# Kernel tuning notes

Hardware: AMD Instinct MI355X
Metric: run time of the kernel (lower is better)

## Reference

```python
import jax, jax.numpy as jnp
import numpy as np

GROUP_SIZE = 64
SHARED_EXPERT_WEIGHT = 1.0
# FP4 E2M1 codebook: sign bit + {0,.5,1,1.5,2,3,4,6}
FP4_TABLE = jnp.array([0.0, 0.5, 1.0, 1.5, 2.0, 3.0, 4.0, 6.0,
                       -0.0, -0.5, -1.0, -1.5, -2.0, -3.0, -4.0, -6.0], dtype=jnp.float32)


def dequant_fp4(packed, scales, group_size=GROUP_SIZE):
    """packed: [..., K//8, N] int32 (8 nibbles along K per word),
    scales: [..., K//group_size, N] -> dequantized [..., K, N] fp32."""
    shifts = (jnp.arange(8, dtype=jnp.int32) * 4)[:, None]          # [8,1]
    nib = jnp.right_shift(packed[..., :, None, :], shifts) & 0xF     # [..., K//8, 8, N]
    w = FP4_TABLE[nib]
    K = packed.shape[-2] * 8
    w = w.reshape(packed.shape[:-2] + (K, packed.shape[-1]))         # [..., K, N]
    s = jnp.repeat(scales, group_size, axis=-2)                      # [..., K, N]
    return w * s


def setup_inputs() -> dict:
    key = jax.random.key(0)
    ks = jax.random.split(key, 12)
    T, K, I, E, TOPK = 2048, 2048, 1024, 8, 2
    GS = GROUP_SIZE
    MAXI = 2**31 - 1
    u = lambda k, shp: jax.random.uniform(k, shp, jnp.float32, 0.005, 0.02)
    probs = jax.random.uniform(ks[10], (T, TOPK), jnp.float32)
    probs = probs / probs.sum(-1, keepdims=True)
    return {
        "hidden_states": jax.random.normal(ks[0], (T, K), jnp.float32),
        "gate_up_weight_packed": jax.random.randint(ks[1], (E, K // 8, 2 * I), 0, MAXI, jnp.int32),
        "gate_up_scales": u(ks[2], (E, K // GS, 2 * I)),
        "down_weight_packed": jax.random.randint(ks[3], (E, I // 8, K), 0, MAXI, jnp.int32),
        "down_scales": u(ks[4], (E, I // GS, K)),
        "shared_gate_up_packed": jax.random.randint(ks[5], (K // 8, 2 * I), 0, MAXI, jnp.int32),
        "shared_gate_up_scales": u(ks[6], (K // GS, 2 * I)),
        "shared_down_packed": jax.random.randint(ks[7], (I // 8, K), 0, MAXI, jnp.int32),
        "shared_down_scales": u(ks[8], (I // GS, K)),
        "expert_ids": jax.random.randint(ks[9], (T, TOPK), 0, E, jnp.int32),
        "expert_probs": probs,
    }


def reference(hidden_states, gate_up_weight_packed, gate_up_scales,
              down_weight_packed, down_scales,
              shared_gate_up_packed, shared_gate_up_scales,
              shared_down_packed, shared_down_scales,
              expert_ids, expert_probs):
    x = hidden_states                                                # [T, K]
    E = gate_up_weight_packed.shape[0]
    # --- routed experts: dequant + grouped GEMM over all tokens per expert ---
    Wgu = dequant_fp4(gate_up_weight_packed, gate_up_scales)         # [E, K, 2I]
    Wd = dequant_fp4(down_weight_packed, down_scales)                # [E, I, K]
    h = jnp.einsum('tk,ekn->etn', x, Wgu)                            # [E, T, 2I]
    gate, up = jnp.split(h, 2, axis=-1)
    act = jax.nn.silu(gate) * up                                     # [E, T, I]
    y = jnp.einsum('eti,eik->etk', act, Wd)                          # [E, T, K]
    # combine[t,e] = sum over top-k slots routed to e of prob
    one_hot = jax.nn.one_hot(expert_ids, E, dtype=x.dtype)           # [T, topk, E]
    combine = jnp.einsum('tk,tke->te', expert_probs, one_hot)        # [T, E]
    out = jnp.einsum('te,etk->tk', combine, y)                       # [T, K]
    # --- shared expert (always applied, weighted) ---
    Wgu_s = dequant_fp4(shared_gate_up_packed, shared_gate_up_scales)  # [K, 2I]
    Wd_s = dequant_fp4(shared_down_packed, shared_down_scales)         # [I, K]
    hs = x @ Wgu_s
    gs, us = jnp.split(hs, 2, axis=-1)
    shared_out = (jax.nn.silu(gs) * us) @ Wd_s
    return out + SHARED_EXPERT_WEIGHT * shared_out
```

## Files before the change

### kernel.cpp

```cpp
#include <hip/hip_runtime.h>
#include <hip/hip_bf16.h>

#define T_TOK 2048
#define K_DIM 2048
#define I_DIM 1024
#define NE    8
#define TOPK  2
#define GS    64

#define NSLOT  (T_TOK * TOPK)
#define TOTROW (NSLOT + T_TOK)
#define MAXTILE 32

typedef __attribute__((ext_vector_type(8))) short short8;
typedef __attribute__((ext_vector_type(4))) float f32x4;

#define WS_XB   ((size_t)65536)
#define WS_ACT  (WS_XB  + (size_t)2048 * 2048 * 2)
#define WS_Y    (WS_ACT + (size_t)TOTROW * 1024 * 2)
#define WS_WGU  (WS_Y   + (size_t)TOTROW * 2048 * 2)
#define WS_WD   (WS_WGU + (size_t)9 * 2048 * 2048 * 2)


__device__ __forceinline__ unsigned pack2(float a, float b) {
    __hip_bfloat162 h = __float22bfloat162_rn(make_float2(a, b));
    return *reinterpret_cast<unsigned*>(&h);
}

__device__ __forceinline__ unsigned scale2(unsigned p, float s) {
    float f0 = __uint_as_float(p << 16) * s;
    float f1 = __uint_as_float(p & 0xFFFF0000u) * s;
    return pack2(f0, f1);
}

__device__ __forceinline__ float bf2f(ushort h) {
    return __uint_as_float((unsigned)h << 16);
}

__device__ __forceinline__ void dq_word(unsigned w, float s, unsigned o[4]) {
    unsigned lo  = w & 0x0F0F0F0Fu;
    unsigned hi  = (w >> 4) & 0x0F0F0F0Fu;
    unsigned mlo = lo & 0x07070707u, mhi = hi & 0x07070707u;
    unsigned Hlo = __builtin_amdgcn_perm(0x40404040u, 0x3F3F3F00u, mlo);
    unsigned Hhi = __builtin_amdgcn_perm(0x40404040u, 0x3F3F3F00u, mhi);
    unsigned Llo = __builtin_amdgcn_perm(0xC0804000u, 0xC0800000u, mlo);
    unsigned Lhi = __builtin_amdgcn_perm(0xC0804000u, 0xC0800000u, mhi);
    Hlo |= (lo & 0x08080808u) << 4;
    Hhi |= (hi & 0x08080808u) << 4;
    unsigned e01 = __builtin_amdgcn_perm(Hlo, Llo, 0x05010400u);
    unsigned e23 = __builtin_amdgcn_perm(Hlo, Llo, 0x07030602u);
    unsigned o01 = __builtin_amdgcn_perm(Hhi, Lhi, 0x05010400u);
    unsigned o23 = __builtin_amdgcn_perm(Hhi, Lhi, 0x07030602u);
    o[0] = scale2(e01, s); o[1] = scale2(e23, s);
    o[2] = scale2(o01, s); o[3] = scale2(o23, s);
}

__device__ __forceinline__ void gld16(const void* g, void* l) {
    __builtin_amdgcn_global_load_lds(
        (const __attribute__((address_space(1))) unsigned*)g,
        (__attribute__((address_space(3))) unsigned*)l, 16, 0, 0);
}

__global__ __launch_bounds__(256) void k_prep_route(
        const float* __restrict__ x, ushort* __restrict__ xb,
        const int* __restrict__ eids, const float* __restrict__ probs,
        int* __restrict__ gcnt, int* __restrict__ gbase,
        int* __restrict__ tok, int* __restrict__ inv) {
    int tid = threadIdx.x;
    int idx = blockIdx.x * 256 + tid;
    const float4* p = (const float4*)(x + (size_t)idx * 8);
    float4 f0 = p[0], f1 = p[1];
    unsigned u0 = pack2(f0.x, f0.z);
    unsigned u1 = pack2(f1.x, f1.z);
    unsigned u2 = pack2(f0.y, f0.w);
    unsigned u3 = pack2(f1.y, f1.w);
    *(int4*)(xb + (size_t)idx * 8) = make_int4(u0, u1, u2, u3);

    if (blockIdx.x == 0) {
        __shared__ int lcnt[NE], lbase[NE], lcur[NE];
        if (tid < NE) lcnt[tid] = 0;
        __syncthreads();
        for (int i = tid; i < NSLOT; i += 256)
            atomicAdd(&lcnt[eids[i]], 1);
        __syncthreads();
        if (tid == 0) {
            int acc = 0;
            for (int e = 0; e < NE; e++) { lbase[e] = acc; acc += lcnt[e]; }
        }
        __syncthreads();
        if (tid < NE) lcur[tid] = lbase[tid];
        __syncthreads();
        for (int i = tid; i < NSLOT; i += 256) {
            int e = eids[i];
            int pos = atomicAdd(&lcur[e], 1);
            tok[pos] = i >> 1;
            inv[i] = pos;
        }
        for (int t = tid; t < T_TOK; t += 256)
            tok[NSLOT + t] = t;
        if (tid < NE) { gcnt[tid] = lcnt[tid]; gbase[tid] = lbase[tid]; }
        if (tid == 0) { gcnt[NE] = T_TOK; gbase[NE] = NSLOT; }
    }
}

__global__ __launch_bounds__(256) void k_dq2(
        const int* __restrict__ gup, const float* __restrict__ gus,
        const int* __restrict__ sup, const float* __restrict__ sus,
        const int* __restrict__ dwp, const float* __restrict__ dsc,
        const int* __restrict__ sdp, const float* __restrict__ sds,
        ushort* __restrict__ wgu_t, ushort* __restrict__ wd_t) {
    int z = blockIdx.z;
    const int* wp; const float* sc; ushort* op; int KW;
    const int N = 2048;
    if (z < 9) {
        KW = 256;
        if (z < NE) { wp = gup + (size_t)z * KW * N; sc = gus + (size_t)z * (KW / 8) * N; }
        else        { wp = sup; sc = sus; }
        op = wgu_t + (size_t)z * KW * 8 * N;
    } else {
        KW = 128;
        int e = z - 9;
        if (blockIdx.x >= 16) return;
        if (e < NE) { wp = dwp + (size_t)e * KW * N; sc = dsc + (size_t)e * (KW / 8) * N; }
        else        { wp = sdp; sc = sds; }
        op = wd_t + (size_t)e * KW * 8 * N;
    }
    int kwt = blockIdx.x * 8 + threadIdx.x;
    int n   = blockIdx.y * 32 + threadIdx.y;
    unsigned w = (unsigned)wp[(size_t)kwt * N + n];
    float s = sc[(size_t)(kwt >> 3) * N + n];
    unsigned o[4]; dq_word(w, s, o);
    *(int4*)(op + (size_t)n * (KW * 8) + kwt * 8) = make_int4(o[0], o[1], o[2], o[3]);
}

__global__ __launch_bounds__(256) void k_gemm_gateup(
        const ushort* __restrict__ xb, const ushort* __restrict__ wgu_t,
        const int* __restrict__ gcnt, const int* __restrict__ gbase,
        const int* __restrict__ tokid, ushort* __restrict__ act) {
    int e = blockIdx.z, cnt = gcnt[e], m0 = blockIdx.y * 128;
    if (m0 >= cnt) return;
    int n0 = blockIdx.x * 64;
    int base = gbase[e];
    const ushort* wt = wgu_t + (size_t)e * 2048 * K_DIM;

    __shared__ __align__(16) ushort xs[128 * 64];
    __shared__ __align__(16) ushort bs[128 * 64];
    __shared__ int ltok[128];

    int tid = threadIdx.x;
    int lane = tid & 63, wv = tid >> 6;
    int lid = lane & 15, quad = lane >> 4;
    int wr = wv >> 1, wc = wv & 1;
    int l8 = lane >> 3, l7 = lane & 7;
    int chunk = (l7 ^ l8) * 8;

    if (tid < 128) ltok[tid] = (m0 + tid < cnt) ? tokid[base + m0 + tid] : 0;
    __syncthreads();

    const ushort* aSrc[4]; const ushort* bSrc[4];
    #pragma unroll
    for (int it = 0; it < 4; it++) {
        int rA = wv * 32 + it * 8 + l8;
        aSrc[it] = xb + (size_t)ltok[rA] * K_DIM + chunk;
        int h = rA >> 6, j = rA & 63;
        int col = (j < 32) ? (n0 + h * 32 + j) : (I_DIM + n0 + h * 32 + (j - 32));
        bSrc[it] = wt + (size_t)col * K_DIM + chunk;
    }

    f32x4 acc[4][4] = {};

    for (int k0 = 0; k0 < K_DIM; k0 += 64) {
        #pragma unroll
        for (int it = 0; it < 4; it++) {
            gld16(aSrc[it] + k0, &xs[(wv * 4 + it) * 512]);
            gld16(bSrc[it] + k0, &bs[(wv * 4 + it) * 512]);
        }
        __syncthreads();
        #pragma unroll
        for (int ks = 0; ks < 2; ks++) {
            int slot = ((ks * 4 + quad) ^ l7) * 8;
            short8 a[4], b[4];
            #pragma unroll
            for (int mt = 0; mt < 4; mt++)
                a[mt] = *(const short8*)&xs[(wr * 64 + mt * 16 + lid) * 64 + slot];
            #pragma unroll
            for (int nt = 0; nt < 4; nt++)
                b[nt] = *(const short8*)&bs[(wc * 64 + nt * 16 + lid) * 64 + slot];
            #pragma unroll
            for (int mt = 0; mt < 4; mt++)
                #pragma unroll
                for (int nt = 0; nt < 4; nt++)
                    acc[mt][nt] = __builtin_amdgcn_mfma_f32_16x16x32_bf16(
                        a[mt], b[nt], acc[mt][nt], 0, 0, 0);
        }
        __syncthreads();
    }

    int c7 = lid & 7;
    int delta = ((c7 >> 1) + ((c7 & 1) << 2)) - c7;
    #pragma unroll
    for (int mt = 0; mt < 4; mt++) {
        #pragma unroll
        for (int i = 0; i < 4; i++) {
            int row = wr * 64 + mt * 16 + quad * 4 + i;
            if (m0 + row < cnt) {
                size_t p = (size_t)(base + m0 + row);
                #pragma unroll
                for (int nt = 0; nt < 2; nt++) {
                    float g = acc[mt][nt][i], u = acc[mt][nt + 2][i];
                    float vv = g / (1.f + __expf(-g)) * u;
                    int ncol = n0 + wc * 32 + nt * 16 + lid;
                    __hip_bfloat16 hb = __float2bfloat16(vv);
                    act[p * I_DIM + ncol + delta] = *reinterpret_cast<ushort*>(&hb);
                }
            }
        }
    }
}

__global__ __launch_bounds__(256) void k_gemm_down(
        const ushort* __restrict__ actb, const ushort* __restrict__ wd_t,
        const int* __restrict__ gcnt, const int* __restrict__ gbase,
        ushort* __restrict__ y) {
    int e = blockIdx.z, cnt = gcnt[e], m0 = blockIdx.y * 128;
    if (m0 >= cnt) return;
    int n0 = blockIdx.x * 128;
    int base = gbase[e];
    const ushort* wt = wd_t + (size_t)e * 2048 * I_DIM;

    __shared__ __align__(16) ushort xs[128 * 64];
    __shared__ __align__(16) ushort bs[128 * 64];

    int tid = threadIdx.x;
    int lane = tid & 63, wv = tid >> 6;
    int lid = lane & 15, quad = lane >> 4;
    int wr = wv >> 1, wc = wv & 1;
    int l8 = lane >> 3, l7 = lane & 7;
    int chunk = (l7 ^ l8) * 8;

    const ushort* aSrc[4]; const ushort* bSrc[4];
    #pragma unroll
    for (int it = 0; it < 4; it++) {
        int rA = wv * 32 + it * 8 + l8;
        int rr = m0 + rA; if (rr >= cnt) rr = cnt - 1;
        aSrc[it] = actb + (size_t)(base + rr) * I_DIM + chunk;
        bSrc[it] = wt + (size_t)(n0 + rA) * I_DIM + chunk;
    }

    f32x4 acc[4][4] = {};

    for (int i0 = 0; i0 < I_DIM; i0 += 64) {
        #pragma unroll
        for (int it = 0; it < 4; it++) {
            gld16(aSrc[it] + i0, &xs[(wv * 4 + it) * 512]);
            gld16(bSrc[it] + i0, &bs[(wv * 4 + it) * 512]);
        }
        __syncthreads();
        #pragma unroll
        for (int ks = 0; ks < 2; ks++) {
            int slot = ((ks * 4 + quad) ^ l7) * 8;
            short8 a[4], b[4];
            #pragma unroll
            for (int mt = 0; mt < 4; mt++)
                a[mt] = *(const short8*)&xs[(wr * 64 + mt * 16 + lid) * 64 + slot];
            #pragma unroll
            for (int nt = 0; nt < 4; nt++)
                b[nt] = *(const short8*)&bs[(wc * 64 + nt * 16 + lid) * 64 + slot];
            #pragma unroll
            for (int mt = 0; mt < 4; mt++)
                #pragma unroll
                for (int nt = 0; nt < 4; nt++)
                    acc[mt][nt] = __builtin_amdgcn_mfma_f32_16x16x32_bf16(
                        a[mt], b[nt], acc[mt][nt], 0, 0, 0);
        }
        __syncthreads();
    }

    #pragma unroll
    for (int mt = 0; mt < 4; mt++) {
        #pragma unroll
        for (int i = 0; i < 4; i++) {
            int row = wr * 64 + mt * 16 + quad * 4 + i;
            if (m0 + row < cnt) {
                ushort* yrow = y + (size_t)(base + m0 + row) * 2048 + n0 + wc * 64 + lid;
                #pragma unroll
                for (int nt = 0; nt < 4; nt++) {
                    __hip_bfloat16 hb = __float2bfloat16(acc[mt][nt][i]);
                    yrow[nt * 16] = *reinterpret_cast<ushort*>(&hb);
                }
            }
        }
    }
}

__global__ __launch_bounds__(256) void k_combine(
        const ushort* __restrict__ y, const int* __restrict__ inv,
        const float* __restrict__ prb, float* __restrict__ out) {
    int idx = blockIdx.x * 256 + threadIdx.x;
    int t = idx >> 8;
    int c = (idx & 255) * 8;
    int p0 = inv[2 * t], p1 = inv[2 * t + 1];
    float w0 = prb[2 * t], w1 = prb[2 * t + 1];
    int4 a = *(const int4*)(y + (size_t)p0 * 2048 + c);
    int4 b = *(const int4*)(y + (size_t)p1 * 2048 + c);
    int4 s = *(const int4*)(y + (size_t)(NSLOT + t) * 2048 + c);
    const ushort* au = (const ushort*)&a;
    const ushort* bu = (const ushort*)&b;
    const ushort* su = (const ushort*)&s;
    float o[8];
    #pragma unroll
    for (int j = 0; j < 8; j++)
        o[j] = w0 * bf2f(au[j]) + w1 * bf2f(bu[j]) + bf2f(su[j]);
    *(float4*)(out + (size_t)t * 2048 + c)     = *(float4*)&o[0];
    *(float4*)(out + (size_t)t * 2048 + c + 4) = *(float4*)&o[4];
}

extern "C" void kernel_launch(void* const* d_in, const int* in_sizes, int n_in,
                              void* d_out, int out_size, void* d_ws, size_t ws_size,
                              hipStream_t stream) {
    const float* x    = (const float*)d_in[0];
    const int*   gup  = (const int*)d_in[1];
    const float* gus  = (const float*)d_in[2];
    const int*   dwp  = (const int*)d_in[3];
    const float* dsc  = (const float*)d_in[4];
    const int*   sup  = (const int*)d_in[5];
    const float* sus  = (const float*)d_in[6];
    const int*   sdp  = (const int*)d_in[7];
    const float* sds  = (const float*)d_in[8];
    const int*   eids = (const int*)d_in[9];
    const float* prb  = (const float*)d_in[10];
    float* out = (float*)d_out;

    char*   ws    = (char*)d_ws;
    int*    gcnt  = (int*)(ws + 0);
    int*    gbase = (int*)(ws + 64);
    int*    tok   = (int*)(ws + 128);
    int*    inv   = (int*)(ws + 24704);
    ushort* xb    = (ushort*)(ws + WS_XB);
    ushort* act   = (ushort*)(ws + WS_ACT);
    ushort* y     = (ushort*)(ws + WS_Y);
    ushort* wgu_t = (ushort*)(ws + WS_WGU);
    ushort* wd_t  = (ushort*)(ws + WS_WD);

    k_prep_route<<<(T_TOK * K_DIM / 8) / 256, 256, 0, stream>>>(
        x, xb, eids, prb, gcnt, gbase, tok, inv);
    k_dq2<<<dim3(32, 64, 18), dim3(8, 32), 0, stream>>>(
        gup, gus, sup, sus, dwp, dsc, sdp, sds, wgu_t, wd_t);
    k_gemm_gateup<<<dim3(I_DIM / 64, MAXTILE, NE + 1), 256, 0, stream>>>(
        xb, wgu_t, gcnt, gbase, tok, act);
    k_gemm_down<<<dim3(K_DIM / 128, MAXTILE, NE + 1), 256, 0, stream>>>(
        act, wd_t, gcnt, gbase, y);
    k_combine<<<(T_TOK * K_DIM / 8) / 256, 256, 0, stream>>>(y, inv, prb, out);
}
```

Baseline: 262.0 us.

## Merge prep and dequant kernels and compact GEMM grids via tile list

Fuses the bf16 conversion, routing and the FP4 weight dequantization into one front kernel, removing a launch and letting the independent pieces share one grid. The routing block now builds a compact list of (expert, m-offset) tiles so the grouped GEMMs launch a 2D grid of at most 55 items instead of 9x32 mostly-empty blocks. This cuts early-exit block scheduling overhead but adds an indirection read per block, and the single routing block still serializes its work inside the merged kernel.

```diff
diff --git a/kernel.cpp b/kernel.cpp
--- a/kernel.cpp
+++ b/kernel.cpp
@@ -10,7 +10,7 @@
 
 #define NSLOT  (T_TOK * TOPK)
 #define TOTROW (NSLOT + T_TOK)
-#define MAXTILE 32
+#define MAXITEM 55
 
 typedef __attribute__((ext_vector_type(8))) short short8;
 typedef __attribute__((ext_vector_type(4))) float f32x4;
@@ -61,22 +61,60 @@
         (__attribute__((address_space(3))) unsigned*)l, 16, 0, 0);
 }
 
-__global__ __launch_bounds__(256) void k_prep_route(
+#define GU_BLK  (9 * 2048)
+#define DN_BLK  (9 * 1024)
+#define PREP_BLK 2048
+#define FRONT_GRID (GU_BLK + DN_BLK + PREP_BLK + 1)
+
+__global__ __launch_bounds__(256) void k_front(
         const float* __restrict__ x, ushort* __restrict__ xb,
+        const int* __restrict__ gup, const float* __restrict__ gus,
+        const int* __restrict__ sup, const float* __restrict__ sus,
+        const int* __restrict__ dwp, const float* __restrict__ dsc,
+        const int* __restrict__ sdp, const float* __restrict__ sds,
+        ushort* __restrict__ wgu_t, ushort* __restrict__ wd_t,
         const int* __restrict__ eids, const float* __restrict__ probs,
         int* __restrict__ gcnt, int* __restrict__ gbase,
+        int* __restrict__ tileCnt, int* __restrict__ tileE, int* __restrict__ tileM,
         int* __restrict__ tok, int* __restrict__ inv) {
+    int id = blockIdx.x;
     int tid = threadIdx.x;
-    int idx = blockIdx.x * 256 + tid;
-    const float4* p = (const float4*)(x + (size_t)idx * 8);
-    float4 f0 = p[0], f1 = p[1];
-    unsigned u0 = pack2(f0.x, f0.z);
-    unsigned u1 = pack2(f1.x, f1.z);
-    unsigned u2 = pack2(f0.y, f0.w);
-    unsigned u3 = pack2(f1.y, f1.w);
-    *(int4*)(xb + (size_t)idx * 8) = make_int4(u0, u1, u2, u3);
-
-    if (blockIdx.x == 0) {
+
+    if (id < GU_BLK + DN_BLK) {
+        const int* wp; const float* sc; ushort* op; int KW, kwt;
+        const int N = 2048;
+        int tx = tid & 7, ty = tid >> 3;
+        int n;
+        if (id < GU_BLK) {
+            int e = id >> 11, rem = id & 2047;
+            int bx = rem & 31, by = rem >> 5;
+            KW = 256; kwt = bx * 8 + tx; n = by * 32 + ty;
+            if (e < NE) { wp = gup + (size_t)e * KW * N; sc = gus + (size_t)e * (KW / 8) * N; }
+            else        { wp = sup; sc = sus; }
+            op = wgu_t + (size_t)e * KW * 8 * N;
+        } else {
+            int id2 = id - GU_BLK;
+            int e = id2 >> 10, rem = id2 & 1023;
+            int bx = rem & 15, by = rem >> 4;
+            KW = 128; kwt = bx * 8 + tx; n = by * 32 + ty;
+            if (e < NE) { wp = dwp + (size_t)e * KW * N; sc = dsc + (size_t)e * (KW / 8) * N; }
+            else        { wp = sdp; sc = sds; }
+            op = wd_t + (size_t)e * KW * 8 * N;
+        }
+        unsigned w = (unsigned)wp[(size_t)kwt * N + n];
+        float s = sc[(size_t)(kwt >> 3) * N + n];
+        unsigned o[4]; dq_word(w, s, o);
+        *(int4*)(op + (size_t)n * (KW * 8) + kwt * 8) = make_int4(o[0], o[1], o[2], o[3]);
+    } else if (id < GU_BLK + DN_BLK + PREP_BLK) {
+        int idx = (id - GU_BLK - DN_BLK) * 256 + tid;
+        const float4* p = (const float4*)(x + (size_t)idx * 8);
+        float4 f0 = p[0], f1 = p[1];
+        unsigned u0 = pack2(f0.x, f0.z);
+        unsigned u1 = pack2(f1.x, f1.z);
+        unsigned u2 = pack2(f0.y, f0.w);
+        unsigned u3 = pack2(f1.y, f1.w);
+        *(int4*)(xb + (size_t)idx * 8) = make_int4(u0, u1, u2, u3);
+    } else {
         __shared__ int lcnt[NE], lbase[NE], lcur[NE];
         if (tid < NE) lcnt[tid] = 0;
         __syncthreads();
@@ -99,48 +137,30 @@
         for (int t = tid; t < T_TOK; t += 256)
             tok[NSLOT + t] = t;
         if (tid < NE) { gcnt[tid] = lcnt[tid]; gbase[tid] = lbase[tid]; }
-        if (tid == 0) { gcnt[NE] = T_TOK; gbase[NE] = NSLOT; }
-    }
-}
-
-__global__ __launch_bounds__(256) void k_dq2(
-        const int* __restrict__ gup, const float* __restrict__ gus,
-        const int* __restrict__ sup, const float* __restrict__ sus,
-        const int* __restrict__ dwp, const float* __restrict__ dsc,
-        const int* __restrict__ sdp, const float* __restrict__ sds,
-        ushort* __restrict__ wgu_t, ushort* __restrict__ wd_t) {
-    int z = blockIdx.z;
-    const int* wp; const float* sc; ushort* op; int KW;
-    const int N = 2048;
-    if (z < 9) {
-        KW = 256;
-        if (z < NE) { wp = gup + (size_t)z * KW * N; sc = gus + (size_t)z * (KW / 8) * N; }
-        else        { wp = sup; sc = sus; }
-        op = wgu_t + (size_t)z * KW * 8 * N;
-    } else {
-        KW = 128;
-        int e = z - 9;
-        if (blockIdx.x >= 16) return;
-        if (e < NE) { wp = dwp + (size_t)e * KW * N; sc = dsc + (size_t)e * (KW / 8) * N; }
-        else        { wp = sdp; sc = sds; }
-        op = wd_t + (size_t)e * KW * 8 * N;
-    }
-    int kwt = blockIdx.x * 8 + threadIdx.x;
-    int n   = blockIdx.y * 32 + threadIdx.y;
-    unsigned w = (unsigned)wp[(size_t)kwt * N + n];
-    float s = sc[(size_t)(kwt >> 3) * N + n];
-    unsigned o[4]; dq_word(w, s, o);
-    *(int4*)(op + (size_t)n * (KW * 8) + kwt * 8) = make_int4(o[0], o[1], o[2], o[3]);
+        if (tid == 0) {
+            gcnt[NE] = T_TOK; gbase[NE] = NSLOT;
+            int nt = 0;
+            for (int e = 0; e < NE + 1; e++) {
+                int c = (e < NE) ? lcnt[e] : T_TOK;
+                for (int m = 0; m < c; m += 128) { tileE[nt] = e; tileM[nt] = m; nt++; }
+            }
+            *tileCnt = nt;
+            for (int i = nt; i < 64; i++) { tileE[i] = 0; tileM[i] = 0; }
+        }
+    }
 }
 
 __global__ __launch_bounds__(256) void k_gemm_gateup(
         const ushort* __restrict__ xb, const ushort* __restrict__ wgu_t,
         const int* __restrict__ gcnt, const int* __restrict__ gbase,
+        const int* __restrict__ tileCnt, const int* __restrict__ tileE,
+        const int* __restrict__ tileM,
         const int* __restrict__ tokid, ushort* __restrict__ act) {
-    int e = blockIdx.z, cnt = gcnt[e], m0 = blockIdx.y * 128;
-    if (m0 >= cnt) return;
+    int item = blockIdx.y;
+    if (item >= *tileCnt) return;
+    int e = tileE[item], m0 = tileM[item];
+    int cnt = gcnt[e], base = gbase[e];
     int n0 = blockIdx.x * 64;
-    int base = gbase[e];
     const ushort* wt = wgu_t + (size_t)e * 2048 * K_DIM;
 
     __shared__ __align__(16) ushort xs[128 * 64];
@@ -221,11 +241,14 @@
 __global__ __launch_bounds__(256) void k_gemm_down(
         const ushort* __restrict__ actb, const ushort* __restrict__ wd_t,
         const int* __restrict__ gcnt, const int* __restrict__ gbase,
+        const int* __restrict__ tileCnt, const int* __restrict__ tileE,
+        const int* __restrict__ tileM,
         ushort* __restrict__ y) {
-    int e = blockIdx.z, cnt = gcnt[e], m0 = blockIdx.y * 128;
-    if (m0 >= cnt) return;
+    int item = blockIdx.y;
+    if (item >= *tileCnt) return;
+    int e = tileE[item], m0 = tileM[item];
+    int cnt = gcnt[e], base = gbase[e];
     int n0 = blockIdx.x * 128;
-    int base = gbase[e];
     const ushort* wt = wd_t + (size_t)e * 2048 * I_DIM;
 
     __shared__ __align__(16) ushort xs[128 * 64];
@@ -331,24 +354,26 @@
     const float* prb  = (const float*)d_in[10];
     float* out = (float*)d_out;
 
-    char*   ws    = (char*)d_ws;
-    int*    gcnt  = (int*)(ws + 0);
-    int*    gbase = (int*)(ws + 64);
-    int*    tok   = (int*)(ws + 128);
-    int*    inv   = (int*)(ws + 24704);
-    ushort* xb    = (ushort*)(ws + WS_XB);
-    ushort* act   = (ushort*)(ws + WS_ACT);
-    ushort* y     = (ushort*)(ws + WS_Y);
-    ushort* wgu_t = (ushort*)(ws + WS_WGU);
-    ushort* wd_t  = (ushort*)(ws + WS_WD);
-
-    k_prep_route<<<(T_TOK * K_DIM / 8) / 256, 256, 0, stream>>>(
-        x, xb, eids, prb, gcnt, gbase, tok, inv);
-    k_dq2<<<dim3(32, 64, 18), dim3(8, 32), 0, stream>>>(
-        gup, gus, sup, sus, dwp, dsc, sdp, sds, wgu_t, wd_t);
-    k_gemm_gateup<<<dim3(I_DIM / 64, MAXTILE, NE + 1), 256, 0, stream>>>(
-        xb, wgu_t, gcnt, gbase, tok, act);
-    k_gemm_down<<<dim3(K_DIM / 128, MAXTILE, NE + 1), 256, 0, stream>>>(
-        act, wd_t, gcnt, gbase, y);
+    char*   ws      = (char*)d_ws;
+    int*    gcnt    = (int*)(ws + 0);
+    int*    gbase   = (int*)(ws + 64);
+    int*    tileCnt = (int*)(ws + 128);
+    int*    tileE   = (int*)(ws + 192);
+    int*    tileM   = (int*)(ws + 448);
+    int*    tok     = (int*)(ws + 1024);
+    int*    inv     = (int*)(ws + 25600);
+    ushort* xb      = (ushort*)(ws + WS_XB);
+    ushort* act     = (ushort*)(ws + WS_ACT);
+    ushort* y       = (ushort*)(ws + WS_Y);
+    ushort* wgu_t   = (ushort*)(ws + WS_WGU);
+    ushort* wd_t    = (ushort*)(ws + WS_WD);
+
+    k_front<<<FRONT_GRID, 256, 0, stream>>>(
+        x, xb, gup, gus, sup, sus, dwp, dsc, sdp, sds, wgu_t, wd_t,
+        eids, prb, gcnt, gbase, tileCnt, tileE, tileM, tok, inv);
+    k_gemm_gateup<<<dim3(I_DIM / 64, MAXITEM), 256, 0, stream>>>(
+        xb, wgu_t, gcnt, gbase, tileCnt, tileE, tileM, tok, act);
+    k_gemm_down<<<dim3(K_DIM / 128, MAXITEM), 256, 0, stream>>>(
+        act, wd_t, gcnt, gbase, tileCnt, tileE, tileM, y);
     k_combine<<<(T_TOK * K_DIM / 8) / 256, 256, 0, stream>>>(y, inv, prb, out);
 }
```

After: 262.3 us. No clear change (+0.1%).
